# Performance work log

Measured on AMD Instinct MI355X. Metric: run time of the kernel, lower is better.

Reference implementation:

```python
import jax, jax.numpy as jnp
import numpy as np
import math

B, L, S, D, H = 4, 2048, 2048, 1024, 16

def setup_inputs() -> dict:
    key = jax.random.key(0)
    ks = jax.random.split(key, 7)
    s = 0.02
    return {
        "queries": jax.random.normal(ks[0], (B, L, D), jnp.float32),
        "keys": jax.random.normal(ks[1], (B, S, D), jnp.float32),
        "values": jax.random.normal(ks[2], (B, S, D), jnp.float32),
        "Wq": jax.random.normal(ks[3], (D, D), jnp.float32) * s,
        "Wk": jax.random.normal(ks[4], (D, D), jnp.float32) * s,
        "Wv": jax.random.normal(ks[5], (D, D), jnp.float32) * s,
        "Wo": jax.random.normal(ks[6], (D, D), jnp.float32) * s,
    }

def _split_heads(x):
    # [B, T, D] -> [B, H, T, d_head]
    b, t, _ = x.shape
    return x.reshape(b, t, H, D // H).transpose(0, 2, 1, 3)

def reference(queries, keys, values, Wq, Wk, Wv, Wo):
    # torch nn.Linear: y = x @ W.T; dropout is identity (p=0 / eval)
    q = _split_heads(queries @ Wq.T)   # [B,H,L,dh]
    k = _split_heads(keys @ Wk.T)      # [B,H,S,dh]
    v = _split_heads(values @ Wv.T)    # [B,H,S,dh]
    dh = q.shape[-1]
    scores = jnp.einsum('bhld,bhsd->bhls', q, k) / math.sqrt(dh)
    causal = jnp.tril(jnp.ones((L, S), dtype=bool))
    scores = jnp.where(causal, scores, -jnp.inf)
    attn = jax.nn.softmax(scores, axis=-1)
    out = jnp.einsum('bhls,bhsd->bhld', attn, v)   # [B,H,L,dh]
    out = out.transpose(0, 2, 1, 3).reshape(B, L, D)
    return out @ Wo.T
```

## Files before the change

### kernel.cpp

```cpp
#include <hip/hip_runtime.h>
#include <hip/hip_bf16.h>
#include <stdint.h>

typedef __bf16 bf16_t;
typedef __bf16 bf16x4 __attribute__((ext_vector_type(4)));
typedef __bf16 bf16x8 __attribute__((ext_vector_type(8)));
typedef float  f32x4  __attribute__((ext_vector_type(4)));
typedef float  f32x16 __attribute__((ext_vector_type(16)));
typedef unsigned int u32;

#define B_  4
#define L_  2048
#define D_  1024
#define H_  16
#define DH_ 64

__device__ __forceinline__ void async_load16(const bf16_t* g, bf16_t* lds) {
    __builtin_amdgcn_global_load_lds(
        (__attribute__((address_space(1))) void*)g,
        (__attribute__((address_space(3))) void*)lds, 16, 0, 0);
}

__global__ __launch_bounds__(256) void cvt4_f32_bf16(
    const float* __restrict__ w0, const float* __restrict__ w1,
    const float* __restrict__ w2, const float* __restrict__ w3,
    bf16_t* __restrict__ o0, bf16_t* __restrict__ o1,
    bf16_t* __restrict__ o2, bf16_t* __restrict__ o3)
{
    int i = blockIdx.x * 256 + threadIdx.x;
    int which = i >> 18;
    int j = (i & 262143) * 4;
    const float* w = which == 0 ? w0 : which == 1 ? w1 : which == 2 ? w2 : w3;
    bf16_t*      o = which == 0 ? o0 : which == 1 ? o1 : which == 2 ? o2 : o3;
    f32x4 v = *(const f32x4*)(w + j);
    bf16x4 ov;
    ov[0] = (bf16_t)v[0]; ov[1] = (bf16_t)v[1];
    ov[2] = (bf16_t)v[2]; ov[3] = (bf16_t)v[3];
    *(bf16x4*)(o + j) = ov;
}

__global__ __launch_bounds__(256) void cvt3_f32_bf16(
    const float* __restrict__ a0, const float* __restrict__ a1,
    const float* __restrict__ a2,
    bf16_t* __restrict__ o0, bf16_t* __restrict__ o1, bf16_t* __restrict__ o2)
{
    int i = blockIdx.x * 256 + threadIdx.x;
    int which = i >> 21;
    size_t j = (size_t)(i & ((1 << 21) - 1)) * 4;
    const float* a = which == 0 ? a0 : which == 1 ? a1 : a2;
    bf16_t*      o = which == 0 ? o0 : which == 1 ? o1 : o2;
    f32x4 v = *(const f32x4*)(a + j);
    bf16x4 ov;
    ov[0] = (bf16_t)v[0]; ov[1] = (bf16_t)v[1];
    ov[2] = (bf16_t)v[2]; ov[3] = (bf16_t)v[3];
    *(bf16x4*)(o + j) = ov;
}

__device__ __forceinline__ void gemm_bt_body(
    const bf16_t* __restrict__ A, const bf16_t* __restrict__ Bm,
    bf16_t* __restrict__ Cb, float* __restrict__ Cf,
    int N, int K, int mode, bf16_t* lds)
{
    const int t = threadIdx.x;
    const int w = t >> 6, l = t & 63;
    const int quad = l >> 4, l15 = l & 15;
    const int wm = w >> 1, wn = w & 1;
    const int rowBase = blockIdx.y * 128;
    const int colBase = blockIdx.x * 128;

    f32x4 acc[4][4] = {};

    for (int k0 = 0; k0 < K; k0 += 32) {
        #pragma unroll
        for (int q2 = 0; q2 < 2; ++q2) {
            int c = q2 * 256 + w * 64 + l;
            int r = c >> 2, kc = c & 3;
            async_load16(&A[(size_t)(rowBase + r) * K + k0 + kc * 8],
                         &lds[(q2 * 256 + w * 64) * 8]);
            async_load16(&Bm[(size_t)(colBase + r) * K + k0 + kc * 8],
                         &lds[4096 + (q2 * 256 + w * 64) * 8]);
        }
        __syncthreads();

        bf16x8 af[4], bfr[4];
        #pragma unroll
        for (int i = 0; i < 4; ++i) {
            af[i]  = *(const bf16x8*)&lds[(wm * 64 + i * 16 + l15) * 32 + quad * 8];
            bfr[i] = *(const bf16x8*)&lds[4096 + (wn * 64 + i * 16 + l15) * 32 + quad * 8];
        }
        #pragma unroll
        for (int mt = 0; mt < 4; ++mt)
            #pragma unroll
            for (int nt = 0; nt < 4; ++nt)
                acc[mt][nt] = __builtin_amdgcn_mfma_f32_16x16x32_bf16(
                    af[mt], bfr[nt], acc[mt][nt], 0, 0, 0);
        __syncthreads();
    }

    #pragma unroll
    for (int mt = 0; mt < 4; ++mt)
        #pragma unroll
        for (int nt = 0; nt < 4; ++nt)
            #pragma unroll
            for (int r = 0; r < 4; ++r) {
                int row = rowBase + wm * 64 + mt * 16 + quad * 4 + r;
                int col = colBase + wn * 64 + nt * 16 + l15;
                float v = acc[mt][nt][r];
                if (mode == 0) {
                    Cb[(size_t)row * N + col] = (bf16_t)v;
                } else if (mode == 1) {
                    int b = row >> 11, s = row & 2047;
                    int h = col >> 6,  d = col & 63;
                    Cb[(((size_t)((b * H_ + h) * DH_ + d)) << 11) + s] = (bf16_t)v;
                } else {
                    Cf[(size_t)row * N + col] = v;
                }
            }
}

__global__ __launch_bounds__(256) void gemm_bt(
    const bf16_t* __restrict__ A, const bf16_t* __restrict__ Bm,
    bf16_t* __restrict__ Cb, float* __restrict__ Cf,
    int M, int N, int K, int mode)
{
    __shared__ __align__(16) bf16_t lds[8192];
    (void)M;
    gemm_bt_body(A, Bm, Cb, Cf, N, K, mode, lds);
}

__global__ __launch_bounds__(256) void gemm_qkv(
    const bf16_t* __restrict__ A0, const bf16_t* __restrict__ B0, bf16_t* __restrict__ C0,
    const bf16_t* __restrict__ A1, const bf16_t* __restrict__ B1, bf16_t* __restrict__ C1,
    const bf16_t* __restrict__ A2, const bf16_t* __restrict__ B2, bf16_t* __restrict__ C2,
    int N, int K)
{
    __shared__ __align__(16) bf16_t lds[8192];
    const int z = blockIdx.z;
    const bf16_t* A  = z == 0 ? A0 : z == 1 ? A1 : A2;
    const bf16_t* Bm = z == 0 ? B0 : z == 1 ? B1 : B2;
    bf16_t*       C  = z == 0 ? C0 : z == 1 ? C1 : C2;
    gemm_bt_body(A, Bm, C, nullptr, N, K, z == 2 ? 1 : 0, lds);
}

__device__ __forceinline__ u32 pack2(float a, float b) {
    union { u32 u; bf16_t h[2]; } p;
    p.h[0] = (bf16_t)a; p.h[1] = (bf16_t)b;
    return p.u;
}

__device__ __forceinline__ void stage_kv(
    const bf16_t* __restrict__ Kw, const bf16_t* __restrict__ Vt,
    bf16_t* kl, bf16_t* vl, int b, int h, int j0, int w, int l)
{
    #pragma unroll
    for (int q2 = 0; q2 < 2; ++q2) {
        int c  = q2 * 256 + w * 64 + l;
        int rr = c >> 3, kc = c & 7;
        int kcs = kc ^ (rr & 7);
        async_load16(&Kw[(size_t)(b * L_ + j0 + rr) * D_ + h * DH_ + kcs * 8],
                     &kl[(q2 * 256 + w * 64) * 8]);
        async_load16(&Vt[((size_t)((b * H_ + h) * DH_ + rr)) * (size_t)L_ + j0 + kcs * 8],
                     &vl[(q2 * 256 + w * 64) * 8]);
    }
}

__global__ __launch_bounds__(256) void attn_fwd(
    const bf16_t* __restrict__ Qw, const bf16_t* __restrict__ Kw,
    const bf16_t* __restrict__ Vt, bf16_t* __restrict__ Ow)
{
    __shared__ __align__(16) bf16_t k_lds[2][4096];
    __shared__ __align__(16) bf16_t v_lds[2][4096];
    __shared__ float l_scr[4][32];

    const int t = threadIdx.x;
    const int w = t >> 6, l = t & 63;
    const int l31 = l & 31, hi = l >> 5;
    const int pr = blockIdx.x;
    const int h = blockIdx.y, b = blockIdx.z;

    #pragma unroll 1
    for (int pass = 0; pass < 2; ++pass) {
        const int qt = pass == 0 ? (15 - pr) : pr;
        const int qrow = qt * 128 + w * 32 + l31;

        bf16x8 bq[4];
        {
            const bf16_t* qp = Qw + (size_t)(b * L_ + qrow) * D_ + h * DH_ + hi * 8;
            #pragma unroll
            for (int kd = 0; kd < 4; ++kd) {
                bq[kd] = *(const bf16x8*)(qp + kd * 16);
                #pragma unroll
                for (int j = 0; j < 8; ++j)
                    bq[kd][j] = (bf16_t)((float)bq[kd][j] * 0.180336880f);
            }
        }

        f32x16 acc0 = {}, acc1 = {};
        float m_i = -1e30f, l_i = 0.f;

        stage_kv(Kw, Vt, k_lds[0], v_lds[0], b, h, 0, w, l);
        __syncthreads();

        const int nkt  = 2 * qt + 2;
        const int wmax = qt * 128 + w * 32 + 31;
        int cur = 0;
        for (int jt = 0; jt < nkt; ++jt) {
            if (jt + 1 < nkt)
                stage_kv(Kw, Vt, k_lds[cur ^ 1], v_lds[cur ^ 1], b, h, (jt + 1) * 64, w, l);

            const int j0 = jt * 64;
            if (j0 <= wmax) {
                f32x16 s0 = {}, s1 = {};
                #pragma unroll
                for (int kd = 0; kd < 4; ++kd) {
                    int sw = ((kd * 2 + hi) ^ (l31 & 7)) * 8;
                    bf16x8 ak0 = *(const bf16x8*)&k_lds[cur][l31 * 64 + sw];
                    bf16x8 ak1 = *(const bf16x8*)&k_lds[cur][(32 + l31) * 64 + sw];
                    s0 = __builtin_amdgcn_mfma_f32_32x32x16_bf16(ak0, bq[kd], s0, 0, 0, 0);
                    s1 = __builtin_amdgcn_mfma_f32_32x32x16_bf16(ak1, bq[kd], s1, 0, 0, 0);
                }

                if (jt >= 2 * qt) {
                    #pragma unroll
                    for (int reg = 0; reg < 16; ++reg) {
                        int row = (reg & 3) + 8 * (reg >> 2) + 4 * hi;
                        if (j0 + row > qrow)      s0[reg] = -1e30f;
                        if (j0 + 32 + row > qrow) s1[reg] = -1e30f;
                    }
                }

                float mt_[16];
                #pragma unroll
                for (int r = 0; r < 16; ++r) mt_[r] = fmaxf(s0[r], s1[r]);
                #pragma unroll
                for (int st = 8; st > 0; st >>= 1)
                    #pragma unroll
                    for (int r = 0; r < st; ++r) mt_[r] = fmaxf(mt_[r], mt_[r + st]);
                float mx = fmaxf(mt_[0], __shfl_xor(mt_[0], 32));

                int grew = !(mx <= m_i + 8.f);
                if (__any(grew)) {
                    float mn = fmaxf(m_i, mx);
                    float alpha = exp2f(m_i - mn);
                    m_i = mn; l_i *= alpha;
                    l_scr[w][l31] = alpha;
                    asm volatile("s_waitcnt lgkmcnt(0)" ::: "memory");
                    #pragma unroll
                    for (int reg = 0; reg < 16; ++reg) {
                        int row = (reg & 3) + 8 * (reg >> 2) + 4 * hi;
                        float a2 = l_scr[w][row];
                        acc0[reg] *= a2; acc1[reg] *= a2;
                    }
                }

                #pragma unroll
                for (int r = 0; r < 16; ++r) s0[r] = exp2f(s0[r] - m_i);
                #pragma unroll
                for (int r = 0; r < 16; ++r) s1[r] = exp2f(s1[r] - m_i);
                float st_[16];
                #pragma unroll
                for (int r = 0; r < 16; ++r) st_[r] = s0[r] + s1[r];
                #pragma unroll
                for (int st = 8; st > 0; st >>= 1)
                    #pragma unroll
                    for (int r = 0; r < st; ++r) st_[r] += st_[r + st];
                l_i += st_[0] + __shfl_xor(st_[0], 32);

                #pragma unroll
                for (int ks = 0; ks < 4; ++ks) {
                    float e0, e1, e2, e3, e4, e5, e6, e7;
                    if (ks == 0)      { e0=s0[0]; e1=s0[1]; e2=s0[2];  e3=s0[3];
                                        e4=s0[4]; e5=s0[5]; e6=s0[6];  e7=s0[7]; }
                    else if (ks == 1) { e0=s0[8]; e1=s0[9]; e2=s0[10]; e3=s0[11];
                                        e4=s0[12];e5=s0[13];e6=s0[14]; e7=s0[15]; }
                    else if (ks == 2) { e0=s1[0]; e1=s1[1]; e2=s1[2];  e3=s1[3];
                                        e4=s1[4]; e5=s1[5]; e6=s1[6];  e7=s1[7]; }
                    else              { e0=s1[8]; e1=s1[9]; e2=s1[10]; e3=s1[11];
                                        e4=s1[12];e5=s1[13];e6=s1[14]; e7=s1[15]; }
                    u32 lo01 = pack2(e0, e1), lo23 = pack2(e2, e3);
                    u32 hi45 = pack2(e4, e5), hi67 = pack2(e6, e7);
                    u32 send0 = hi ? lo01 : hi45;
                    u32 send1 = hi ? lo23 : hi67;
                    u32 recv0 = __shfl_xor(send0, 32);
                    u32 recv1 = __shfl_xor(send1, 32);
                    union { u32 uw[4]; bf16x8 v8; } pu;
                    pu.uw[0] = hi ? recv0 : lo01;
                    pu.uw[1] = hi ? recv1 : lo23;
                    pu.uw[2] = hi ? hi45 : recv0;
                    pu.uw[3] = hi ? hi67 : recv1;

                    int sw = ((ks * 2 + hi) ^ (l31 & 7)) * 8;
                    bf16x8 bv0 = *(const bf16x8*)&v_lds[cur][l31 * 64 + sw];
                    bf16x8 bv1 = *(const bf16x8*)&v_lds[cur][(32 + l31) * 64 + sw];
                    acc0 = __builtin_amdgcn_mfma_f32_32x32x16_bf16(pu.v8, bv0, acc0, 0, 0, 0);
                    acc1 = __builtin_amdgcn_mfma_f32_32x32x16_bf16(pu.v8, bv1, acc1, 0, 0, 0);
                }
            }

            __syncthreads();
            cur ^= 1;
        }

        l_scr[w][l31] = l_i;
        asm volatile("s_waitcnt lgkmcnt(0)" ::: "memory");
        #pragma unroll
        for (int reg = 0; reg < 16; ++reg) {
            int row = (reg & 3) + 8 * (reg >> 2) + 4 * hi;
            float inv = 1.f / l_scr[w][row];
            int grow = qt * 128 + w * 32 + row;
            size_t base = (size_t)(b * L_ + grow) * D_ + h * DH_ + l31;
            Ow[base]      = (bf16_t)(acc0[reg] * inv);
            Ow[base + 32] = (bf16_t)(acc1[reg] * inv);
        }
    }
}

extern "C" void kernel_launch(void* const* d_in, const int* in_sizes, int n_in,
                              void* d_out, int out_size, void* d_ws, size_t ws_size,
                              hipStream_t stream)
{
    const float* queries = (const float*)d_in[0];
    const float* keys    = (const float*)d_in[1];
    const float* values  = (const float*)d_in[2];
    const float* Wq = (const float*)d_in[3];
    const float* Wk = (const float*)d_in[4];
    const float* Wv = (const float*)d_in[5];
    const float* Wo = (const float*)d_in[6];
    float* out = (float*)d_out;

    const size_t SZ = (size_t)B_ * L_ * D_;
    const size_t WZ = (size_t)D_ * D_;
    bf16_t* cbuf  = (bf16_t*)d_ws;
    bf16_t* cWq   = cbuf + SZ;
    bf16_t* cWk   = cWq + WZ;
    bf16_t* cWv   = cWk + WZ;
    bf16_t* cWo   = cWv + WZ;
    bf16_t* q_ws  = cWo + WZ;
    bf16_t* k_ws  = q_ws + SZ;
    bf16_t* vt_ws = k_ws + SZ;
    bf16_t* a_ws  = cbuf;

    bf16_t* ck = (bf16_t*)d_out;
    bf16_t* cv = ck + SZ;

    dim3 gg(D_ / 128, (B_ * L_) / 128);

    cvt4_f32_bf16<<<4096, 256, 0, stream>>>(Wq, Wk, Wv, Wo, cWq, cWk, cWv, cWo);
    cvt3_f32_bf16<<<24576, 256, 0, stream>>>(queries, keys, values, cbuf, ck, cv);

    gemm_qkv<<<dim3(D_ / 128, (B_ * L_) / 128, 3), 256, 0, stream>>>(
        cbuf, cWq, q_ws,
        ck,   cWk, k_ws,
        cv,   cWv, vt_ws,
        D_, D_);

    attn_fwd<<<dim3(8, H_, B_), 256, 0, stream>>>(q_ws, k_ws, vt_ws, a_ws);

    gemm_bt<<<gg, 256, 0, stream>>>(a_ws, cWo, nullptr, out, B_ * L_, D_, D_, 2);
}
```

Baseline: 381.1 us.

## Use 32x32x16 MFMA with BK=64 swizzled LDS tiles in GEMMs; fuse conversion kernels

The projection GEMMs now stage 64-wide K tiles into a doubled LDS buffer with an XOR swizzle and compute with 32x32x16 bf16 MFMAs instead of 16x16x32. This halves the number of barrier-separated K iterations, cuts LDS bank conflicts and improves operand reuse per MFMA. The two f32-to-bf16 conversion kernels are merged into one launch, and the GEMM dimensions are hardcoded. The cost is more LDS per block, which may reduce occupancy, and the K loop still has no load/compute overlap.

Measured after the change: 366.2 us. 3.9% less time.

```diff
diff --git a/kernel.cpp b/kernel.cpp
--- a/kernel.cpp
+++ b/kernel.cpp
@@ -21,125 +21,136 @@
         (__attribute__((address_space(3))) void*)lds, 16, 0, 0);
 }
 
-__global__ __launch_bounds__(256) void cvt4_f32_bf16(
+__global__ __launch_bounds__(256) void cvt_all(
+    const float* __restrict__ a0, const float* __restrict__ a1,
+    const float* __restrict__ a2,
     const float* __restrict__ w0, const float* __restrict__ w1,
     const float* __restrict__ w2, const float* __restrict__ w3,
-    bf16_t* __restrict__ o0, bf16_t* __restrict__ o1,
-    bf16_t* __restrict__ o2, bf16_t* __restrict__ o3)
+    bf16_t* __restrict__ oa0, bf16_t* __restrict__ oa1, bf16_t* __restrict__ oa2,
+    bf16_t* __restrict__ ow0, bf16_t* __restrict__ ow1,
+    bf16_t* __restrict__ ow2, bf16_t* __restrict__ ow3)
 {
     int i = blockIdx.x * 256 + threadIdx.x;
-    int which = i >> 18;
-    int j = (i & 262143) * 4;
-    const float* w = which == 0 ? w0 : which == 1 ? w1 : which == 2 ? w2 : w3;
-    bf16_t*      o = which == 0 ? o0 : which == 1 ? o1 : which == 2 ? o2 : o3;
-    f32x4 v = *(const f32x4*)(w + j);
+    const float* src; bf16_t* dst; size_t j;
+    if (i < 3 * (1 << 21)) {
+        int which = i >> 21;
+        src = which == 0 ? a0 : which == 1 ? a1 : a2;
+        dst = which == 0 ? oa0 : which == 1 ? oa1 : oa2;
+        j = (size_t)(i & ((1 << 21) - 1)) * 4;
+    } else {
+        int k = i - 3 * (1 << 21);
+        int which = k >> 18;
+        src = which == 0 ? w0 : which == 1 ? w1 : which == 2 ? w2 : w3;
+        dst = which == 0 ? ow0 : which == 1 ? ow1 : which == 2 ? ow2 : ow3;
+        j = (size_t)(k & ((1 << 18) - 1)) * 4;
+    }
+    f32x4 v = *(const f32x4*)(src + j);
     bf16x4 ov;
     ov[0] = (bf16_t)v[0]; ov[1] = (bf16_t)v[1];
     ov[2] = (bf16_t)v[2]; ov[3] = (bf16_t)v[3];
-    *(bf16x4*)(o + j) = ov;
-}
-
-__global__ __launch_bounds__(256) void cvt3_f32_bf16(
-    const float* __restrict__ a0, const float* __restrict__ a1,
-    const float* __restrict__ a2,
-    bf16_t* __restrict__ o0, bf16_t* __restrict__ o1, bf16_t* __restrict__ o2)
-{
-    int i = blockIdx.x * 256 + threadIdx.x;
-    int which = i >> 21;
-    size_t j = (size_t)(i & ((1 << 21) - 1)) * 4;
-    const float* a = which == 0 ? a0 : which == 1 ? a1 : a2;
-    bf16_t*      o = which == 0 ? o0 : which == 1 ? o1 : o2;
-    f32x4 v = *(const f32x4*)(a + j);
-    bf16x4 ov;
-    ov[0] = (bf16_t)v[0]; ov[1] = (bf16_t)v[1];
-    ov[2] = (bf16_t)v[2]; ov[3] = (bf16_t)v[3];
-    *(bf16x4*)(o + j) = ov;
+    *(bf16x4*)(dst + j) = ov;
+}
+
+__device__ __forceinline__ void stage_ab(
+    const bf16_t* __restrict__ A, const bf16_t* __restrict__ Bm,
+    bf16_t* lds, int rowBase, int colBase, int k0, int t)
+{
+    const int wbase = t & ~63;
+    #pragma unroll
+    for (int sweep = 0; sweep < 4; ++sweep) {
+        int c = sweep * 256 + t;
+        int r = c >> 3, kc = c & 7;
+        int kcs = kc ^ (r & 7);
+        async_load16(&A[((size_t)(rowBase + r) << 10) + k0 + kcs * 8],
+                     &lds[(sweep * 256 + wbase) * 8]);
+        async_load16(&Bm[((size_t)(colBase + r) << 10) + k0 + kcs * 8],
+                     &lds[8192 + (sweep * 256 + wbase) * 8]);
+    }
 }
 
 __device__ __forceinline__ void gemm_bt_body(
     const bf16_t* __restrict__ A, const bf16_t* __restrict__ Bm,
     bf16_t* __restrict__ Cb, float* __restrict__ Cf,
-    int N, int K, int mode, bf16_t* lds)
+    int mode, bf16_t* lds)
 {
     const int t = threadIdx.x;
     const int w = t >> 6, l = t & 63;
-    const int quad = l >> 4, l15 = l & 15;
+    const int l31 = l & 31, hi = l >> 5;
     const int wm = w >> 1, wn = w & 1;
     const int rowBase = blockIdx.y * 128;
     const int colBase = blockIdx.x * 128;
 
-    f32x4 acc[4][4] = {};
-
-    for (int k0 = 0; k0 < K; k0 += 32) {
+    f32x16 acc[2][2] = {};
+
+    for (int k0 = 0; k0 < 1024; k0 += 64) {
+        stage_ab(A, Bm, lds, rowBase, colBase, k0, t);
+        __syncthreads();
+
         #pragma unroll
-        for (int q2 = 0; q2 < 2; ++q2) {
-            int c = q2 * 256 + w * 64 + l;
-            int r = c >> 2, kc = c & 3;
-            async_load16(&A[(size_t)(rowBase + r) * K + k0 + kc * 8],
-                         &lds[(q2 * 256 + w * 64) * 8]);
-            async_load16(&Bm[(size_t)(colBase + r) * K + k0 + kc * 8],
-                         &lds[4096 + (q2 * 256 + w * 64) * 8]);
+        for (int ks = 0; ks < 4; ++ks) {
+            int g = ks * 2 + hi;
+            bf16x8 af[2], bg[2];
+            #pragma unroll
+            for (int mf = 0; mf < 2; ++mf) {
+                int row = wm * 64 + mf * 32 + l31;
+                af[mf] = *(const bf16x8*)&lds[row * 64 + ((g ^ (row & 7)) * 8)];
+            }
+            #pragma unroll
+            for (int nf = 0; nf < 2; ++nf) {
+                int row = wn * 64 + nf * 32 + l31;
+                bg[nf] = *(const bf16x8*)&lds[8192 + row * 64 + ((g ^ (row & 7)) * 8)];
+            }
+            #pragma unroll
+            for (int mf = 0; mf < 2; ++mf)
+                #pragma unroll
+                for (int nf = 0; nf < 2; ++nf)
+                    acc[mf][nf] = __builtin_amdgcn_mfma_f32_32x32x16_bf16(
+                        af[mf], bg[nf], acc[mf][nf], 0, 0, 0);
         }
         __syncthreads();
-
-        bf16x8 af[4], bfr[4];
+    }
+
+    #pragma unroll
+    for (int mf = 0; mf < 2; ++mf)
         #pragma unroll
-        for (int i = 0; i < 4; ++i) {
-            af[i]  = *(const bf16x8*)&lds[(wm * 64 + i * 16 + l15) * 32 + quad * 8];
-            bfr[i] = *(const bf16x8*)&lds[4096 + (wn * 64 + i * 16 + l15) * 32 + quad * 8];
-        }
-        #pragma unroll
-        for (int mt = 0; mt < 4; ++mt)
-            #pragma unroll
-            for (int nt = 0; nt < 4; ++nt)
-                acc[mt][nt] = __builtin_amdgcn_mfma_f32_16x16x32_bf16(
-                    af[mt], bfr[nt], acc[mt][nt], 0, 0, 0);
-        __syncthreads();
-    }
-
-    #pragma unroll
-    for (int mt = 0; mt < 4; ++mt)
-        #pragma unroll
-        for (int nt = 0; nt < 4; ++nt)
-            #pragma unroll
-            for (int r = 0; r < 4; ++r) {
-                int row = rowBase + wm * 64 + mt * 16 + quad * 4 + r;
-                int col = colBase + wn * 64 + nt * 16 + l15;
-                float v = acc[mt][nt][r];
+        for (int nf = 0; nf < 2; ++nf)
+            #pragma unroll
+            for (int reg = 0; reg < 16; ++reg) {
+                int row = rowBase + wm * 64 + mf * 32
+                        + (reg & 3) + 8 * (reg >> 2) + 4 * hi;
+                int col = colBase + wn * 64 + nf * 32 + l31;
+                float v = acc[mf][nf][reg];
                 if (mode == 0) {
-                    Cb[(size_t)row * N + col] = (bf16_t)v;
+                    Cb[((size_t)row << 10) + col] = (bf16_t)v;
                 } else if (mode == 1) {
                     int b = row >> 11, s = row & 2047;
                     int h = col >> 6,  d = col & 63;
                     Cb[(((size_t)((b * H_ + h) * DH_ + d)) << 11) + s] = (bf16_t)v;
                 } else {
-                    Cf[(size_t)row * N + col] = v;
+                    Cf[((size_t)row << 10) + col] = v;
                 }
             }
 }
 
 __global__ __launch_bounds__(256) void gemm_bt(
     const bf16_t* __restrict__ A, const bf16_t* __restrict__ Bm,
-    bf16_t* __restrict__ Cb, float* __restrict__ Cf,
-    int M, int N, int K, int mode)
-{
-    __shared__ __align__(16) bf16_t lds[8192];
-    (void)M;
-    gemm_bt_body(A, Bm, Cb, Cf, N, K, mode, lds);
+    bf16_t* __restrict__ Cb, float* __restrict__ Cf, int mode)
+{
+    __shared__ __align__(16) bf16_t lds[16384];
+    gemm_bt_body(A, Bm, Cb, Cf, mode, lds);
 }
 
 __global__ __launch_bounds__(256) void gemm_qkv(
     const bf16_t* __restrict__ A0, const bf16_t* __restrict__ B0, bf16_t* __restrict__ C0,
     const bf16_t* __restrict__ A1, const bf16_t* __restrict__ B1, bf16_t* __restrict__ C1,
-    const bf16_t* __restrict__ A2, const bf16_t* __restrict__ B2, bf16_t* __restrict__ C2,
-    int N, int K)
-{
-    __shared__ __align__(16) bf16_t lds[8192];
+    const bf16_t* __restrict__ A2, const bf16_t* __restrict__ B2, bf16_t* __restrict__ C2)
+{
+    __shared__ __align__(16) bf16_t lds[16384];
     const int z = blockIdx.z;
     const bf16_t* A  = z == 0 ? A0 : z == 1 ? A1 : A2;
     const bf16_t* Bm = z == 0 ? B0 : z == 1 ? B1 : B2;
     bf16_t*       C  = z == 0 ? C0 : z == 1 ? C1 : C2;
-    gemm_bt_body(A, Bm, C, nullptr, N, K, z == 2 ? 1 : 0, lds);
+    gemm_bt_body(A, Bm, C, nullptr, z == 2 ? 1 : 0, lds);
 }
 
 __device__ __forceinline__ u32 pack2(float a, float b) {
@@ -343,18 +354,16 @@
     bf16_t* ck = (bf16_t*)d_out;
     bf16_t* cv = ck + SZ;
 
-    dim3 gg(D_ / 128, (B_ * L_) / 128);
-
-    cvt4_f32_bf16<<<4096, 256, 0, stream>>>(Wq, Wk, Wv, Wo, cWq, cWk, cWv, cWo);
-    cvt3_f32_bf16<<<24576, 256, 0, stream>>>(queries, keys, values, cbuf, ck, cv);
+    cvt_all<<<28672, 256, 0, stream>>>(queries, keys, values, Wq, Wk, Wv, Wo,
+                                       cbuf, ck, cv, cWq, cWk, cWv, cWo);
 
     gemm_qkv<<<dim3(D_ / 128, (B_ * L_) / 128, 3), 256, 0, stream>>>(
         cbuf, cWq, q_ws,
         ck,   cWk, k_ws,
-        cv,   cWv, vt_ws,
-        D_, D_);
+        cv,   cWv, vt_ws);
 
     attn_fwd<<<dim3(8, H_, B_), 256, 0, stream>>>(q_ws, k_ws, vt_ws, a_ws);
 
-    gemm_bt<<<gg, 256, 0, stream>>>(a_ws, cWo, nullptr, out, B_ * L_, D_, D_, 2);
-}
+    gemm_bt<<<dim3(D_ / 128, (B_ * L_) / 128), 256, 0, stream>>>(
+        a_ws, cWo, nullptr, out, 2);
+}
```
